# Kernel tuning notes

Measured on AMD Instinct MI355X. Metric: run time of the kernel, lower is better.

The kernel has to match this reference:

```python
import jax, jax.numpy as jnp
import numpy as np

B, S, D, L = 4, 512, 768, 64


def setup_inputs() -> dict:
    key = jax.random.key(0)
    k1, k2, k3, k4, k5 = jax.random.split(key, 5)
    return {
        "head": jax.random.normal(k1, (B, S, D), dtype=jnp.float32),
        "dep": jax.random.normal(k2, (B, S, D), dtype=jnp.float32),
        "label_U_diag": jax.random.normal(k3, (L, D), dtype=jnp.float32) * 0.02,
        "label_W": jax.random.normal(k4, (L, 2 * D), dtype=jnp.float32) * 0.02,
        "label_b": jax.random.normal(k5, (L,), dtype=jnp.float32) * 0.02,
    }


def reference(head, dep, label_U_diag, label_W, label_b):
    # t1[b,l,i,o] = sum_d head[b,i,d] * U[l,d] * dep[b,o,d]  (diag bilinear)
    t1 = jnp.einsum('bid,ld,bod->blio', head, label_U_diag, dep)
    # Linear term: instead of materializing the O(S^2 * 2D) concat tensor,
    # split W into head/dep halves and broadcast-add two O(S*L) matmuls.
    d = head.shape[-1]
    Wh, Wd = label_W[:, :d], label_W[:, d:]
    t2_h = jnp.einsum('bid,ld->bli', head, Wh)  # [B, L, S] (row / head index)
    t2_d = jnp.einsum('bod,ld->blo', dep, Wd)   # [B, L, S] (col / dep index)
    return t1 + t2_h[:, :, :, None] + t2_d[:, :, None, :] + label_b[None, :, None, None]
```

## Files before the change

### kernel.cpp

```cpp
#include <hip/hip_runtime.h>

typedef __bf16 bf16;
typedef __bf16 bf16x8 __attribute__((ext_vector_type(8)));
typedef float  f32x4  __attribute__((ext_vector_type(4)));

#define S 512
#define DD 768
#define LL 64
#define BB 4

__device__ __forceinline__ void async_copy16(const void* g, void* l) {
    __builtin_amdgcn_global_load_lds(
        (const __attribute__((address_space(1))) unsigned int*)g,
        (__attribute__((address_space(3))) unsigned int*)l,
        16, 0, 0);
}

__device__ __forceinline__ bf16x8 scale_cvt(float4 a, float4 b, float4 ua, float4 ub) {
    bf16x8 p;
    p[0] = (bf16)(a.x * ua.x); p[1] = (bf16)(a.y * ua.y);
    p[2] = (bf16)(a.z * ua.z); p[3] = (bf16)(a.w * ua.w);
    p[4] = (bf16)(b.x * ub.x); p[5] = (bf16)(b.y * ub.y);
    p[6] = (bf16)(b.z * ub.z); p[7] = (bf16)(b.w * ub.w);
    return p;
}

__global__ void cvt_dep_kernel(const float* __restrict__ dep, bf16* __restrict__ out) {
    int idx = (blockIdx.x * 256 + threadIdx.x) * 8;
    float4 a = *(const float4*)(dep + idx);
    float4 c = *(const float4*)(dep + idx + 4);
    bf16x8 p;
    p[0] = (bf16)a.x; p[1] = (bf16)a.y; p[2] = (bf16)a.z; p[3] = (bf16)a.w;
    p[4] = (bf16)c.x; p[5] = (bf16)c.y; p[6] = (bf16)c.z; p[7] = (bf16)c.w;
    *(bf16x8*)(out + idx) = p;
}

__global__ void t2_kernel(const float* __restrict__ head, const float* __restrict__ dep,
                          const float* __restrict__ W, const float* __restrict__ bias,
                          float* __restrict__ t2h, float* __restrict__ t2d) {
    __shared__ float Wl[16][DD];
    __shared__ float red[64][4][16];
    int bid = blockIdx.x;
    int sel = bid >> 7;
    int r   = bid & 127;
    int b   = r >> 5;
    int lg  = (r >> 3) & 3;
    int ic  = r & 7;
    const float* src = sel ? dep : head;
    int t = threadIdx.x;

    for (int l16 = 0; l16 < 16; ++l16) {
        const float* wp = W + (size_t)(lg * 16 + l16) * (2 * DD) + sel * DD;
        Wl[l16][t]       = wp[t];
        Wl[l16][t + 256] = wp[t + 256];
        Wl[l16][t + 512] = wp[t + 512];
    }
    __syncthreads();

    int iq = t >> 2, dq = t & 3;
    int i  = ic * 64 + iq;
    const float* rowp = src + (size_t)(b * S + i) * DD;
    float acc[16];
#pragma unroll
    for (int l16 = 0; l16 < 16; ++l16) acc[l16] = 0.f;
    for (int it = 0; it < 48; ++it) {
        int d = dq * 4 + it * 16;
        float4 x = *(const float4*)(rowp + d);
#pragma unroll
        for (int l16 = 0; l16 < 16; ++l16) {
            float4 wv = *(const float4*)&Wl[l16][d];
            acc[l16] += x.x * wv.x + x.y * wv.y + x.z * wv.z + x.w * wv.w;
        }
    }
#pragma unroll
    for (int l16 = 0; l16 < 16; ++l16) red[iq][dq][l16] = acc[l16];
    __syncthreads();

    int iq2 = t >> 2, l4 = t & 3;
    float* dst = sel ? t2d : t2h;
#pragma unroll
    for (int j = 0; j < 4; ++j) {
        int l16 = l4 * 4 + j;
        float v = red[iq2][0][l16] + red[iq2][1][l16] + red[iq2][2][l16] + red[iq2][3][l16];
        if (sel) v += bias[lg * 16 + l16];
        dst[(size_t)(b * LL + lg * 16 + l16) * S + ic * 64 + iq2] = v;
    }
}

__global__ __launch_bounds__(256, 5) void biaffine_main(
    const float* __restrict__ head, const bf16* __restrict__ depb,
    const float* __restrict__ U, const float* __restrict__ t2h,
    const float* __restrict__ t2d, float* __restrict__ out) {
    __shared__ __align__(16) bf16 As[2][128][32];
    __shared__ __align__(16) bf16 Bs[2][128][32];

    const int tid  = threadIdx.x;
    const int lane = tid & 63;
    const int w    = tid >> 6;
    const int bi0  = (blockIdx.x & 3) << 7;
    const int bo0  = (blockIdx.x >> 2) << 7;
    const int l    = blockIdx.y;
    const int b    = blockIdx.z;

    bf16* AsB = &As[0][0][0];
    bf16* BsB = &Bs[0][0][0];

    const int r1 = tid >> 2;
    const int cp = tid & 3;
    const int sw = (r1 >> 1) & 3;
    const int ca = cp ^ sw;
    const float* hp0 = head + (size_t)(b * S + bi0 + r1) * DD + ca * 8;
    const float* hp1 = hp0 + (size_t)64 * DD;
    const float* Up  = U + (size_t)l * DD + ca * 8;
    const int aoff0 = r1 * 32 + cp * 8;
    const int aoff1 = (r1 + 64) * 32 + cp * 8;

    const int rB0 = w * 32 + (lane >> 2);
    const int rB1 = rB0 + 16;
    const int cpB = lane & 3;
    const bf16* bg0 = depb + (size_t)(b * S + bo0 + rB0) * DD + (cpB ^ ((rB0 >> 1) & 3)) * 8;
    const bf16* bg1 = depb + (size_t)(b * S + bo0 + rB1) * DD + (cpB ^ ((rB1 >> 1) & 3)) * 8;
    const int boff0 = (w * 32) * 32;
    const int boff1 = (w * 32 + 16) * 32;

    const int wr = w & 1, wc = w >> 1;
    const int mrow = lane & 15, q = lane >> 4;
    int aFo[4], bFo[4];
#pragma unroll
    for (int mi = 0; mi < 4; ++mi) {
        int rowA = wr * 64 + mi * 16 + mrow;
        aFo[mi] = rowA * 32 + ((q ^ ((rowA >> 1) & 3)) * 8);
        int rowB = wc * 64 + mi * 16 + mrow;
        bFo[mi] = rowB * 32 + ((q ^ ((rowB >> 1) & 3)) * 8);
    }

    f32x4 acc[4][4];
#pragma unroll
    for (int mi = 0; mi < 4; ++mi)
#pragma unroll
        for (int ni = 0; ni < 4; ++ni)
            acc[mi][ni] = (f32x4){0.f, 0.f, 0.f, 0.f};

    async_copy16(bg0, BsB + boff0);
    async_copy16(bg1, BsB + boff1);
    float4 h0a = *(const float4*)(hp0);
    float4 h0b = *(const float4*)(hp0 + 4);
    float4 h1a = *(const float4*)(hp1);
    float4 h1b = *(const float4*)(hp1 + 4);
    float4 uA  = *(const float4*)(Up);
    float4 uB  = *(const float4*)(Up + 4);
    *(bf16x8*)(AsB + aoff0) = scale_cvt(h0a, h0b, uA, uB);
    *(bf16x8*)(AsB + aoff1) = scale_cvt(h1a, h1b, uA, uB);
    __syncthreads();

    for (int kt = 0; kt < 24; ++kt) {
        const int coff = (kt & 1) * 4096;
        const int soff = coff ^ 4096;
        const bool st = kt < 23;

        if (st) {
            async_copy16(bg0 + (kt + 1) * 32, BsB + soff + boff0);
            async_copy16(bg1 + (kt + 1) * 32, BsB + soff + boff1);
            const float* h0 = hp0 + (kt + 1) * 32;
            const float* h1 = hp1 + (kt + 1) * 32;
            h0a = *(const float4*)(h0);
            h0b = *(const float4*)(h0 + 4);
            h1a = *(const float4*)(h1);
            h1b = *(const float4*)(h1 + 4);
            uA  = *(const float4*)(Up + (kt + 1) * 32);
            uB  = *(const float4*)(Up + (kt + 1) * 32 + 4);
        }

        bf16x8 af[4], bfr[4];
#pragma unroll
        for (int mi = 0; mi < 4; ++mi) af[mi]  = *(const bf16x8*)(AsB + coff + aFo[mi]);
#pragma unroll
        for (int ni = 0; ni < 4; ++ni) bfr[ni] = *(const bf16x8*)(BsB + coff + bFo[ni]);
#pragma unroll
        for (int mi = 0; mi < 4; ++mi)
#pragma unroll
            for (int ni = 0; ni < 4; ++ni)
                acc[mi][ni] = __builtin_amdgcn_mfma_f32_16x16x32_bf16(af[mi], bfr[ni], acc[mi][ni], 0, 0, 0);

        if (st) {
            *(bf16x8*)(AsB + soff + aoff0) = scale_cvt(h0a, h0b, uA, uB);
            *(bf16x8*)(AsB + soff + aoff1) = scale_cvt(h1a, h1b, uA, uB);
        }
        __syncthreads();
    }

    const size_t bl = (size_t)(b * LL + l);
    const float* t2hp = t2h + bl * S + bi0 + wr * 64;
    const float* t2dp = t2d + bl * S + bo0 + wc * 64;
    float* outbase = out + bl * (size_t)(S * S);
#pragma unroll
    for (int mi = 0; mi < 4; ++mi) {
        float4 th = *(const float4*)&t2hp[mi * 16 + q * 4];
        int row0 = bi0 + wr * 64 + mi * 16 + q * 4;
#pragma unroll
        for (int ni = 0; ni < 4; ++ni) {
            int col = bo0 + wc * 64 + ni * 16 + mrow;
            float td = t2dp[ni * 16 + mrow];
            float* op = outbase + (size_t)row0 * S + col;
            op[0 * S] = acc[mi][ni][0] + th.x + td;
            op[1 * S] = acc[mi][ni][1] + th.y + td;
            op[2 * S] = acc[mi][ni][2] + th.z + td;
            op[3 * S] = acc[mi][ni][3] + th.w + td;
        }
    }
}

extern "C" void kernel_launch(void* const* d_in, const int* in_sizes, int n_in,
                              void* d_out, int out_size, void* d_ws, size_t ws_size,
                              hipStream_t stream) {
    const float* head = (const float*)d_in[0];
    const float* dep  = (const float*)d_in[1];
    const float* U    = (const float*)d_in[2];
    const float* W    = (const float*)d_in[3];
    const float* bias = (const float*)d_in[4];
    float* out = (float*)d_out;

    char*  ws   = (char*)d_ws;
    bf16*  depb = (bf16*)ws;
    float* t2h  = (float*)(ws + 3145728);
    float* t2d  = (float*)(ws + 3145728 + 524288);

    cvt_dep_kernel<<<768, 256, 0, stream>>>(dep, depb);
    t2_kernel<<<256, 256, 0, stream>>>(head, dep, W, bias, t2h, t2d);
    biaffine_main<<<dim3(16, LL, BB), 256, 0, stream>>>(head, depb, U, t2h, t2d, out);
}
```

Baseline: 469.5 us.

## Load scaled head A-fragments directly into registers, bypassing LDS staging

The A operand (head scaled by U, converted to bf16) is no longer staged through shared memory. Each lane now loads the exact fp32 elements its MFMA fragment needs straight from global memory and converts them in registers. This removes the A-tile LDS writes and reads and halves shared-memory use. In exchange, each wave loads its own 64-row slice of head, so the two waves sharing a row block load the same data twice, and register pressure rises; the occupancy hint is lowered from 5 to 3 to allow this.

Result: slower. 653.8 us (+39.3%).

```diff
diff --git a/kernel.cpp b/kernel.cpp
--- a/kernel.cpp
+++ b/kernel.cpp
@@ -87,11 +87,10 @@
     }
 }
 
-__global__ __launch_bounds__(256, 5) void biaffine_main(
+__global__ __launch_bounds__(256, 3) void biaffine_main(
     const float* __restrict__ head, const bf16* __restrict__ depb,
     const float* __restrict__ U, const float* __restrict__ t2h,
     const float* __restrict__ t2d, float* __restrict__ out) {
-    __shared__ __align__(16) bf16 As[2][128][32];
     __shared__ __align__(16) bf16 Bs[2][128][32];
 
     const int tid  = threadIdx.x;
@@ -102,18 +101,7 @@
     const int l    = blockIdx.y;
     const int b    = blockIdx.z;
 
-    bf16* AsB = &As[0][0][0];
     bf16* BsB = &Bs[0][0][0];
-
-    const int r1 = tid >> 2;
-    const int cp = tid & 3;
-    const int sw = (r1 >> 1) & 3;
-    const int ca = cp ^ sw;
-    const float* hp0 = head + (size_t)(b * S + bi0 + r1) * DD + ca * 8;
-    const float* hp1 = hp0 + (size_t)64 * DD;
-    const float* Up  = U + (size_t)l * DD + ca * 8;
-    const int aoff0 = r1 * 32 + cp * 8;
-    const int aoff1 = (r1 + 64) * 32 + cp * 8;
 
     const int rB0 = w * 32 + (lane >> 2);
     const int rB1 = rB0 + 16;
@@ -125,14 +113,19 @@
 
     const int wr = w & 1, wc = w >> 1;
     const int mrow = lane & 15, q = lane >> 4;
-    int aFo[4], bFo[4];
-#pragma unroll
-    for (int mi = 0; mi < 4; ++mi) {
-        int rowA = wr * 64 + mi * 16 + mrow;
-        aFo[mi] = rowA * 32 + ((q ^ ((rowA >> 1) & 3)) * 8);
-        int rowB = wc * 64 + mi * 16 + mrow;
-        bFo[mi] = rowB * 32 + ((q ^ ((rowB >> 1) & 3)) * 8);
-    }
+
+    int bFo[4];
+#pragma unroll
+    for (int ni = 0; ni < 4; ++ni) {
+        int rowB = wc * 64 + ni * 16 + mrow;
+        bFo[ni] = rowB * 32 + ((q ^ ((rowB >> 1) & 3)) * 8);
+    }
+
+    const float* hA0 = head + (size_t)(b * S + bi0 + wr * 64 +  0 + mrow) * DD + q * 8;
+    const float* hA1 = head + (size_t)(b * S + bi0 + wr * 64 + 16 + mrow) * DD + q * 8;
+    const float* hA2 = head + (size_t)(b * S + bi0 + wr * 64 + 32 + mrow) * DD + q * 8;
+    const float* hA3 = head + (size_t)(b * S + bi0 + wr * 64 + 48 + mrow) * DD + q * 8;
+    const float* Upl = U + (size_t)l * DD + q * 8;
 
     f32x4 acc[4][4];
 #pragma unroll
@@ -143,14 +136,11 @@
 
     async_copy16(bg0, BsB + boff0);
     async_copy16(bg1, BsB + boff1);
-    float4 h0a = *(const float4*)(hp0);
-    float4 h0b = *(const float4*)(hp0 + 4);
-    float4 h1a = *(const float4*)(hp1);
-    float4 h1b = *(const float4*)(hp1 + 4);
-    float4 uA  = *(const float4*)(Up);
-    float4 uB  = *(const float4*)(Up + 4);
-    *(bf16x8*)(AsB + aoff0) = scale_cvt(h0a, h0b, uA, uB);
-    *(bf16x8*)(AsB + aoff1) = scale_cvt(h1a, h1b, uA, uB);
+    float4 hP0a = *(const float4*)(hA0);     float4 hP0b = *(const float4*)(hA0 + 4);
+    float4 hP1a = *(const float4*)(hA1);     float4 hP1b = *(const float4*)(hA1 + 4);
+    float4 hP2a = *(const float4*)(hA2);     float4 hP2b = *(const float4*)(hA2 + 4);
+    float4 hP3a = *(const float4*)(hA3);     float4 hP3b = *(const float4*)(hA3 + 4);
+    float4 uPa  = *(const float4*)(Upl);     float4 uPb  = *(const float4*)(Upl + 4);
     __syncthreads();
 
     for (int kt = 0; kt < 24; ++kt) {
@@ -158,34 +148,33 @@
         const int soff = coff ^ 4096;
         const bool st = kt < 23;
 
+        bf16x8 af[4];
+        af[0] = scale_cvt(hP0a, hP0b, uPa, uPb);
+        af[1] = scale_cvt(hP1a, hP1b, uPa, uPb);
+        af[2] = scale_cvt(hP2a, hP2b, uPa, uPb);
+        af[3] = scale_cvt(hP3a, hP3b, uPa, uPb);
+
         if (st) {
             async_copy16(bg0 + (kt + 1) * 32, BsB + soff + boff0);
             async_copy16(bg1 + (kt + 1) * 32, BsB + soff + boff1);
-            const float* h0 = hp0 + (kt + 1) * 32;
-            const float* h1 = hp1 + (kt + 1) * 32;
-            h0a = *(const float4*)(h0);
-            h0b = *(const float4*)(h0 + 4);
-            h1a = *(const float4*)(h1);
-            h1b = *(const float4*)(h1 + 4);
-            uA  = *(const float4*)(Up + (kt + 1) * 32);
-            uB  = *(const float4*)(Up + (kt + 1) * 32 + 4);
+            const int ko = (kt + 1) * 32;
+            hP0a = *(const float4*)(hA0 + ko); hP0b = *(const float4*)(hA0 + ko + 4);
+            hP1a = *(const float4*)(hA1 + ko); hP1b = *(const float4*)(hA1 + ko + 4);
+            hP2a = *(const float4*)(hA2 + ko); hP2b = *(const float4*)(hA2 + ko + 4);
+            hP3a = *(const float4*)(hA3 + ko); hP3b = *(const float4*)(hA3 + ko + 4);
+            uPa  = *(const float4*)(Upl + ko); uPb  = *(const float4*)(Upl + ko + 4);
         }
 
-        bf16x8 af[4], bfr[4];
-#pragma unroll
-        for (int mi = 0; mi < 4; ++mi) af[mi]  = *(const bf16x8*)(AsB + coff + aFo[mi]);
+        bf16x8 bfr[4];
 #pragma unroll
         for (int ni = 0; ni < 4; ++ni) bfr[ni] = *(const bf16x8*)(BsB + coff + bFo[ni]);
+
 #pragma unroll
         for (int mi = 0; mi < 4; ++mi)
 #pragma unroll
             for (int ni = 0; ni < 4; ++ni)
                 acc[mi][ni] = __builtin_amdgcn_mfma_f32_16x16x32_bf16(af[mi], bfr[ni], acc[mi][ni], 0, 0, 0);
 
-        if (st) {
-            *(bf16x8*)(AsB + soff + aoff0) = scale_cvt(h0a, h0b, uA, uB);
-            *(bf16x8*)(AsB + soff + aoff1) = scale_cvt(h1a, h1b, uA, uB);
-        }
         __syncthreads();
     }
 
```
